# Optimization experiments

Measured on AMD Instinct MI355X. Metric: run time of the kernel, lower is better.

## Reference

```python
import jax, jax.numpy as jnp
import numpy as np

# quantization formats
E_Q, M_Q = 4, 3      # E4M3 fp8 for input/param quantizers
E_A, M_A = 5, 10     # fp16-like accumulate / output format


def quant(x, exp, man):
    """Round-to-nearest-even float quantization to (exp, man) bits,
    with subnormals and saturation (mptorch float_quantize semantics)."""
    ebias = 2 ** (exp - 1) - 1
    emin = 1 - ebias                      # min normal exponent
    maxv = (2.0 - 2.0 ** (-man)) * 2.0 ** ebias
    ax = jnp.abs(x)
    e = jnp.floor(jnp.log2(jnp.where(ax > 0, ax, 1.0)))
    e = jnp.maximum(e, emin)              # subnormal range shares emin scale
    scale = jnp.exp2(man - e)
    q = jnp.round(x * scale) / scale      # jnp.round is half-to-even
    return jnp.clip(q, -maxv, maxv)


def qgemm(x, wt, exp_add, man_add):
    """Custom-precision GEMM x[M,K] @ wt[K,N] with fma=True:
    the running accumulator is requantized to (exp_add, man_add)
    after every rank-1 (per-k) fused multiply-add."""
    M, K = x.shape
    N = wt.shape[1]

    def step(acc, xw):
        xk, wk = xw                       # [M], [N]
        acc = quant(acc + xk[:, None] * wk[None, :], exp_add, man_add)
        return acc, None

    acc0 = jnp.zeros((M, N), x.dtype)
    acc, _ = jax.lax.scan(step, acc0, (x.T, wt))
    return acc


def setup_inputs() -> dict:
    key = jax.random.key(0)
    k1, k2, k3 = jax.random.split(key, 3)
    in_f, out_f, m = 1024, 1024, 2048
    x = jax.random.normal(k1, (m, in_f), jnp.float32)
    weight = jax.random.normal(k2, (out_f, in_f), jnp.float32) / np.float32(np.sqrt(in_f))
    bound = 1.0 / np.float32(np.sqrt(in_f))
    bias = jax.random.uniform(k3, (out_f,), jnp.float32, -bound, bound)
    return {"x": x, "weight": weight, "bias": bias}


def reference(x, weight, bias):
    qx = quant(x, E_Q, M_Q)               # input_quant
    qw = quant(weight, E_Q, M_Q)          # param_quant
    qb = quant(bias, E_Q, M_Q)            # param_quant
    out = qgemm(qx, qw.T, E_A, M_A)       # float_gemm with fma accumulation
    out = out + qb[None, :]
    out = quant(out, E_A, M_A)            # output requantization
    return out
```

## Files before the change

kernel.cpp:

```cpp
#include <hip/hip_runtime.h>
#include <hip/hip_fp16.h>


#define M_DIM 2048
#define N_DIM 1024
#define K_DIM 1024

#define BM 64
#define BN 64
#define BK 64
#define NCHUNK (K_DIM / BK)

typedef unsigned u32;

__device__ __forceinline__ float quant_e4m3(float v) {
  unsigned au = __float_as_uint(v) & 0x7fffffffu;
  if (au == 0u) return v;
  int e = (int)(au >> 23) - 127;
  if (e < -6) e = -6;
  float s  = __uint_as_float((unsigned)(130 - e) << 23);
  float is = __uint_as_float((unsigned)(124 + e) << 23);
  float r = rintf(v * s) * is;
  return fminf(240.f, fmaxf(-240.f, r));
}

__global__ __launch_bounds__(256) void prep_kernel(const float* __restrict__ x,
                                                   const float* __restrict__ w,
                                                   u32* __restrict__ xP,
                                                   u32* __restrict__ wP) {
  __shared__ float tile[32][33];
  const int tx = threadIdx.x & 31;
  const int ty = threadIdx.x >> 5;
  if (blockIdx.x < 2048) {
    const int c0 = (blockIdx.x & 31) * 32;
    const int r0 = (blockIdx.x >> 5) * 32;
#pragma unroll
    for (int i = 0; i < 4; i++) {
      int r = r0 + ty + i * 8;
      tile[ty + i * 8][tx] = quant_e4m3(x[(size_t)r * K_DIM + c0 + tx]);
    }
    __syncthreads();
#pragma unroll
    for (int i = 0; i < 2; i++) {
      int tl = ty + i * 8;
      u32 lo = (u32)__half_as_ushort(__float2half(tile[tx][2 * tl]));
      u32 hi = (u32)__half_as_ushort(__float2half(tile[tx][2 * tl + 1]));
      xP[(size_t)(c0 / 2 + tl) * M_DIM + r0 + tx] = lo | (hi << 16);
    }
  } else {
    const int b = blockIdx.x - 2048;
    const int k0 = (b & 31) * 32;
    const int n0 = (b >> 5) * 32;
#pragma unroll
    for (int i = 0; i < 4; i++) {
      int n = n0 + ty + i * 8;
      tile[ty + i * 8][tx] = quant_e4m3(w[(size_t)n * K_DIM + k0 + tx]);
    }
    __syncthreads();
    const int tpl = threadIdx.x >> 4;
    const int npl = threadIdx.x & 15;
    u32 a0 = (u32)__half_as_ushort(__float2half(tile[2 * npl][2 * tpl])) |
             ((u32)__half_as_ushort(__float2half(tile[2 * npl + 1][2 * tpl])) << 16);
    u32 a1 = (u32)__half_as_ushort(__float2half(tile[2 * npl][2 * tpl + 1])) |
             ((u32)__half_as_ushort(__float2half(tile[2 * npl + 1][2 * tpl + 1])) << 16);
    uint2 o; o.x = a0; o.y = a1;
    *reinterpret_cast<uint2*>(wP + (size_t)(k0 / 2 + tpl) * N_DIM + n0 + 2 * npl) = o;
  }
}


__device__ __forceinline__ void gld16(const void* g, void* l) {
  __builtin_amdgcn_global_load_lds((const __attribute__((address_space(1))) u32*)g,
                                   (__attribute__((address_space(3))) u32*)l, 16, 0, 0);
}

__device__ __forceinline__ void pkfma_lo(u32& acc, u32 x, u32 w) {
  asm("v_pk_fma_f16 %0, %1, %2, %0 op_sel:[0,0,0] op_sel_hi:[0,1,1]"
      : "+v"(acc) : "v"(x), "v"(w));
}
__device__ __forceinline__ void pkfma_hi(u32& acc, u32 x, u32 w) {
  asm("v_pk_fma_f16 %0, %1, %2, %0 op_sel:[1,0,0] op_sel_hi:[1,1,1]"
      : "+v"(acc) : "v"(x), "v"(w));
}

__global__ __launch_bounds__(256, 2) void gemm_qfma(const u32* __restrict__ xP,
                                                    const u32* __restrict__ wP,
                                                    const float* __restrict__ b,
                                                    float* __restrict__ outp) {
  __shared__ __align__(16) u32 xs[2][BK / 2][BM];
  __shared__ __align__(16) u32 ws[2][BK / 2][BN];
  const int tid = threadIdx.x;
  const int lane = tid & 63;
  const int wv = tid >> 6;
  const int wr = wv >> 1;
  const int wc = wv & 1;
  const int tml = lane >> 3;
  const int tnl = lane & 7;
  const int bn0 = blockIdx.x * BN;
  const int bm0 = blockIdx.y * BM;
  const int xoff = wr * 32 + tml * 4;
  const int woff = wc * 32 + tnl * 4;

  u32 acc[4][2];
#pragma unroll
  for (int i = 0; i < 4; i++) { acc[i][0] = 0u; acc[i][1] = 0u; }

  const int srow = tid >> 4;
  const int scol = (tid & 15) << 2;
  const u32* xsrc = xP + (size_t)srow * M_DIM + bm0 + scol;
  const u32* wsrc = wP + (size_t)srow * N_DIM + bn0 + scol;

  auto stage = [&](int ch, int buf) {
    const u32* xp = xsrc + (size_t)ch * (BK / 2) * M_DIM;
    const u32* wp = wsrc + (size_t)ch * (BK / 2) * N_DIM;
    char* xl = (char*)&xs[buf][0][0] + tid * 16;
    char* wl = (char*)&ws[buf][0][0] + tid * 16;
    gld16(xp, xl);
    gld16(xp + (size_t)16 * M_DIM, xl + 4096);
    gld16(wp, wl);
    gld16(wp + (size_t)16 * N_DIM, wl + 4096);
  };

  auto compute = [&](int buf) {
#pragma unroll
    for (int tp = 0; tp < BK / 2; tp++) {
      const uint4 xv = *reinterpret_cast<const uint4*>(&xs[buf][tp][xoff]);
      const uint4 wv4 = *reinterpret_cast<const uint4*>(&ws[buf][tp][woff]);
      pkfma_lo(acc[0][0], xv.x, wv4.x); pkfma_lo(acc[0][1], xv.x, wv4.z);
      pkfma_lo(acc[1][0], xv.y, wv4.x); pkfma_lo(acc[1][1], xv.y, wv4.z);
      pkfma_lo(acc[2][0], xv.z, wv4.x); pkfma_lo(acc[2][1], xv.z, wv4.z);
      pkfma_lo(acc[3][0], xv.w, wv4.x); pkfma_lo(acc[3][1], xv.w, wv4.z);
      pkfma_hi(acc[0][0], xv.x, wv4.y); pkfma_hi(acc[0][1], xv.x, wv4.w);
      pkfma_hi(acc[1][0], xv.y, wv4.y); pkfma_hi(acc[1][1], xv.y, wv4.w);
      pkfma_hi(acc[2][0], xv.z, wv4.y); pkfma_hi(acc[2][1], xv.z, wv4.w);
      pkfma_hi(acc[3][0], xv.w, wv4.y); pkfma_hi(acc[3][1], xv.w, wv4.w);
    }
  };

  stage(0, 0);
  __syncthreads();
#pragma unroll 1
  for (int ch = 0; ch < NCHUNK; ch += 2) {
    stage(ch + 1, 1);
    compute(0);
    __syncthreads();
    if (ch + 2 < NCHUNK) stage(ch + 2, 0);
    compute(1);
    __syncthreads();
  }

  const int nc = bn0 + wc * 32 + tnl * 4;
  float4 bq;
  bq.x = quant_e4m3(b[nc + 0]);
  bq.y = quant_e4m3(b[nc + 1]);
  bq.z = quant_e4m3(b[nc + 2]);
  bq.w = quant_e4m3(b[nc + 3]);
#pragma unroll
  for (int i = 0; i < 4; i++) {
    __half2 a0 = *reinterpret_cast<__half2*>(&acc[i][0]);
    __half2 a1 = *reinterpret_cast<__half2*>(&acc[i][1]);
    float4 o;
    o.x = __half2float(__float2half(__low2float(a0)  + bq.x));
    o.y = __half2float(__float2half(__high2float(a0) + bq.y));
    o.z = __half2float(__float2half(__low2float(a1)  + bq.z));
    o.w = __half2float(__float2half(__high2float(a1) + bq.w));
    *reinterpret_cast<float4*>(
        outp + (size_t)(bm0 + wr * 32 + tml * 4 + i) * N_DIM + nc) = o;
  }
}

extern "C" void kernel_launch(void* const* d_in, const int* in_sizes, int n_in,
                              void* d_out, int out_size, void* d_ws, size_t ws_size,
                              hipStream_t stream) {
  const float* x = (const float*)d_in[0];
  const float* w = (const float*)d_in[1];
  const float* b = (const float*)d_in[2];
  float* outp = (float*)d_out;

  char* ws_ = (char*)d_ws;
  u32* xP = (u32*)ws_;
  u32* wP = (u32*)(ws_ + (size_t)(4 << 20));

  hipLaunchKernelGGL(prep_kernel, dim3(2048 + 1024), dim3(256), 0, stream,
                     x, w, xP, wP);
  hipLaunchKernelGGL(gemm_qfma, dim3(N_DIM / BN, M_DIM / BM), dim3(256), 0, stream,
                     xP, wP, b, outp);
}
```

Baseline: 110.3 us.

## Broadcast x operands through scalar registers and drop x from shared memory

Changes the packed layouts so each wave covers 16 rows of M and each lane one N column. x values become wave-uniform and are loaded with scalar loads straight from global into SGPRs, which are then used as the scalar operand of v_pk_fma_f16. Only the w tile is staged in LDS, as one dword per lane per k-pair. This removes the x LDS traffic and half the ds_read bandwidth. The risk is scalar-load latency sitting on the inner loop without prefetching, and column-strided scalar output stores in place of float4 stores.

```diff
diff --git a/kernel.cpp b/kernel.cpp
--- a/kernel.cpp
+++ b/kernel.cpp
@@ -12,6 +12,7 @@
 #define NCHUNK (K_DIM / BK)
 
 typedef unsigned u32;
+typedef u32 su16 __attribute__((ext_vector_type(16)));
 
 __device__ __forceinline__ float quant_e4m3(float v) {
   unsigned au = __float_as_uint(v) & 0x7fffffffu;
@@ -26,8 +27,8 @@
 
 __global__ __launch_bounds__(256) void prep_kernel(const float* __restrict__ x,
                                                    const float* __restrict__ w,
-                                                   u32* __restrict__ xP,
-                                                   u32* __restrict__ wP) {
+                                                   u32* __restrict__ xQ,
+                                                   u32* __restrict__ wK) {
   __shared__ float tile[32][33];
   const int tx = threadIdx.x & 31;
   const int ty = threadIdx.x >> 5;
@@ -43,9 +44,11 @@
 #pragma unroll
     for (int i = 0; i < 2; i++) {
       int tl = ty + i * 8;
-      u32 lo = (u32)__half_as_ushort(__float2half(tile[tx][2 * tl]));
-      u32 hi = (u32)__half_as_ushort(__float2half(tile[tx][2 * tl + 1]));
-      xP[(size_t)(c0 / 2 + tl) * M_DIM + r0 + tx] = lo | (hi << 16);
+      int mp = tx >> 1;
+      int j = tx & 1;
+      u32 lo = (u32)__half_as_ushort(__float2half(tile[2 * mp][2 * tl + j]));
+      u32 hi = (u32)__half_as_ushort(__float2half(tile[2 * mp + 1][2 * tl + j]));
+      xQ[(size_t)(c0 / 2 + tl) * M_DIM + r0 + tx] = lo | (hi << 16);
     }
   } else {
     const int b = blockIdx.x - 2048;
@@ -57,14 +60,13 @@
       tile[ty + i * 8][tx] = quant_e4m3(w[(size_t)n * K_DIM + k0 + tx]);
     }
     __syncthreads();
-    const int tpl = threadIdx.x >> 4;
-    const int npl = threadIdx.x & 15;
-    u32 a0 = (u32)__half_as_ushort(__float2half(tile[2 * npl][2 * tpl])) |
-             ((u32)__half_as_ushort(__float2half(tile[2 * npl + 1][2 * tpl])) << 16);
-    u32 a1 = (u32)__half_as_ushort(__float2half(tile[2 * npl][2 * tpl + 1])) |
-             ((u32)__half_as_ushort(__float2half(tile[2 * npl + 1][2 * tpl + 1])) << 16);
-    uint2 o; o.x = a0; o.y = a1;
-    *reinterpret_cast<uint2*>(wP + (size_t)(k0 / 2 + tpl) * N_DIM + n0 + 2 * npl) = o;
+#pragma unroll
+    for (int i = 0; i < 2; i++) {
+      int tl = ty + i * 8;
+      u32 lo = (u32)__half_as_ushort(__float2half(tile[tx][2 * tl]));
+      u32 hi = (u32)__half_as_ushort(__float2half(tile[tx][2 * tl + 1]));
+      wK[(size_t)(k0 / 2 + tl) * N_DIM + n0 + tx] = lo | (hi << 16);
+    }
   }
 }
 
@@ -74,66 +76,54 @@
                                    (__attribute__((address_space(3))) u32*)l, 16, 0, 0);
 }
 
-__device__ __forceinline__ void pkfma_lo(u32& acc, u32 x, u32 w) {
-  asm("v_pk_fma_f16 %0, %1, %2, %0 op_sel:[0,0,0] op_sel_hi:[0,1,1]"
-      : "+v"(acc) : "v"(x), "v"(w));
+__device__ __forceinline__ void pk_k0(u32& acc, u32 x, u32 w) {
+  asm("v_pk_fma_f16 %0, %1, %2, %0 op_sel:[0,0,0] op_sel_hi:[1,0,1]"
+      : "+v"(acc) : "s"(x), "v"(w));
 }
-__device__ __forceinline__ void pkfma_hi(u32& acc, u32 x, u32 w) {
-  asm("v_pk_fma_f16 %0, %1, %2, %0 op_sel:[1,0,0] op_sel_hi:[1,1,1]"
-      : "+v"(acc) : "v"(x), "v"(w));
+__device__ __forceinline__ void pk_k1(u32& acc, u32 x, u32 w) {
+  asm("v_pk_fma_f16 %0, %1, %2, %0 op_sel:[0,1,0] op_sel_hi:[1,1,1]"
+      : "+v"(acc) : "s"(x), "v"(w));
 }
 
-__global__ __launch_bounds__(256, 2) void gemm_qfma(const u32* __restrict__ xP,
-                                                    const u32* __restrict__ wP,
+__global__ __launch_bounds__(256, 2) void gemm_qfma(const u32* __restrict__ xQ,
+                                                    const u32* __restrict__ wK,
                                                     const float* __restrict__ b,
                                                     float* __restrict__ outp) {
-  __shared__ __align__(16) u32 xs[2][BK / 2][BM];
-  __shared__ __align__(16) u32 ws[2][BK / 2][BN];
+  __shared__ __align__(16) u32 wsh[2][BK / 2][BN];
   const int tid = threadIdx.x;
   const int lane = tid & 63;
-  const int wv = tid >> 6;
-  const int wr = wv >> 1;
-  const int wc = wv & 1;
-  const int tml = lane >> 3;
-  const int tnl = lane & 7;
+  const int uw = __builtin_amdgcn_readfirstlane(tid >> 6);
   const int bn0 = blockIdx.x * BN;
   const int bm0 = blockIdx.y * BM;
-  const int xoff = wr * 32 + tml * 4;
-  const int woff = wc * 32 + tnl * 4;
 
-  u32 acc[4][2];
+  u32 acc[8];
 #pragma unroll
-  for (int i = 0; i < 4; i++) { acc[i][0] = 0u; acc[i][1] = 0u; }
+  for (int i = 0; i < 8; i++) acc[i] = 0u;
 
-  const int srow = tid >> 4;
-  const int scol = (tid & 15) << 2;
-  const u32* xsrc = xP + (size_t)srow * M_DIM + bm0 + scol;
-  const u32* wsrc = wP + (size_t)srow * N_DIM + bn0 + scol;
-
+  const u32* wsrc = wK + (size_t)(tid >> 4) * N_DIM + bn0 + ((tid & 15) << 2);
   auto stage = [&](int ch, int buf) {
-    const u32* xp = xsrc + (size_t)ch * (BK / 2) * M_DIM;
     const u32* wp = wsrc + (size_t)ch * (BK / 2) * N_DIM;
-    char* xl = (char*)&xs[buf][0][0] + tid * 16;
-    char* wl = (char*)&ws[buf][0][0] + tid * 16;
-    gld16(xp, xl);
-    gld16(xp + (size_t)16 * M_DIM, xl + 4096);
+    char* wl = (char*)&wsh[buf][0][0] + tid * 16;
     gld16(wp, wl);
     gld16(wp + (size_t)16 * N_DIM, wl + 4096);
   };
 
-  auto compute = [&](int buf) {
+  const u32* const xw = xQ + bm0 + uw * 16;
+
+  auto compute = [&](int ch, int buf) {
 #pragma unroll
     for (int tp = 0; tp < BK / 2; tp++) {
-      const uint4 xv = *reinterpret_cast<const uint4*>(&xs[buf][tp][xoff]);
-      const uint4 wv4 = *reinterpret_cast<const uint4*>(&ws[buf][tp][woff]);
-      pkfma_lo(acc[0][0], xv.x, wv4.x); pkfma_lo(acc[0][1], xv.x, wv4.z);
-      pkfma_lo(acc[1][0], xv.y, wv4.x); pkfma_lo(acc[1][1], xv.y, wv4.z);
-      pkfma_lo(acc[2][0], xv.z, wv4.x); pkfma_lo(acc[2][1], xv.z, wv4.z);
-      pkfma_lo(acc[3][0], xv.w, wv4.x); pkfma_lo(acc[3][1], xv.w, wv4.z);
-      pkfma_hi(acc[0][0], xv.x, wv4.y); pkfma_hi(acc[0][1], xv.x, wv4.w);
-      pkfma_hi(acc[1][0], xv.y, wv4.y); pkfma_hi(acc[1][1], xv.y, wv4.w);
-      pkfma_hi(acc[2][0], xv.z, wv4.y); pkfma_hi(acc[2][1], xv.z, wv4.w);
-      pkfma_hi(acc[3][0], xv.w, wv4.y); pkfma_hi(acc[3][1], xv.w, wv4.w);
+      const su16 xv = *reinterpret_cast<const su16*>(
+          xw + (size_t)(ch * (BK / 2) + tp) * M_DIM);
+      const u32 wv = wsh[buf][tp][lane];
+      pk_k0(acc[0], xv[0],  wv); pk_k0(acc[1], xv[2],  wv);
+      pk_k0(acc[2], xv[4],  wv); pk_k0(acc[3], xv[6],  wv);
+      pk_k0(acc[4], xv[8],  wv); pk_k0(acc[5], xv[10], wv);
+      pk_k0(acc[6], xv[12], wv); pk_k0(acc[7], xv[14], wv);
+      pk_k1(acc[0], xv[1],  wv); pk_k1(acc[1], xv[3],  wv);
+      pk_k1(acc[2], xv[5],  wv); pk_k1(acc[3], xv[7],  wv);
+      pk_k1(acc[4], xv[9],  wv); pk_k1(acc[5], xv[11], wv);
+      pk_k1(acc[6], xv[13], wv); pk_k1(acc[7], xv[15], wv);
     }
   };
 
@@ -142,30 +132,21 @@
 #pragma unroll 1
   for (int ch = 0; ch < NCHUNK; ch += 2) {
     stage(ch + 1, 1);
-    compute(0);
+    compute(ch, 0);
     __syncthreads();
     if (ch + 2 < NCHUNK) stage(ch + 2, 0);
-    compute(1);
+    compute(ch + 1, 1);
     __syncthreads();
   }
 
-  const int nc = bn0 + wc * 32 + tnl * 4;
-  float4 bq;
-  bq.x = quant_e4m3(b[nc + 0]);
-  bq.y = quant_e4m3(b[nc + 1]);
-  bq.z = quant_e4m3(b[nc + 2]);
-  bq.w = quant_e4m3(b[nc + 3]);
+  const int nc = bn0 + lane;
+  const float bq = quant_e4m3(b[nc]);
+  float* orow = outp + (size_t)(bm0 + uw * 16) * N_DIM + nc;
 #pragma unroll
-  for (int i = 0; i < 4; i++) {
-    __half2 a0 = *reinterpret_cast<__half2*>(&acc[i][0]);
-    __half2 a1 = *reinterpret_cast<__half2*>(&acc[i][1]);
-    float4 o;
-    o.x = __half2float(__float2half(__low2float(a0)  + bq.x));
-    o.y = __half2float(__float2half(__high2float(a0) + bq.y));
-    o.z = __half2float(__float2half(__low2float(a1)  + bq.z));
-    o.w = __half2float(__float2half(__high2float(a1) + bq.w));
-    *reinterpret_cast<float4*>(
-        outp + (size_t)(bm0 + wr * 32 + tml * 4 + i) * N_DIM + nc) = o;
+  for (int mp = 0; mp < 8; mp++) {
+    __half2 a = *reinterpret_cast<__half2*>(&acc[mp]);
+    orow[(size_t)(2 * mp) * N_DIM]     = __half2float(__float2half(__low2float(a)  + bq));
+    orow[(size_t)(2 * mp + 1) * N_DIM] = __half2float(__float2half(__high2float(a) + bq));
   }
 }
 
@@ -178,11 +159,11 @@
   float* outp = (float*)d_out;
 
   char* ws_ = (char*)d_ws;
-  u32* xP = (u32*)ws_;
-  u32* wP = (u32*)(ws_ + (size_t)(4 << 20));
+  u32* xQ = (u32*)ws_;
+  u32* wK = (u32*)(ws_ + (size_t)(4 << 20));
 
   hipLaunchKernelGGL(prep_kernel, dim3(2048 + 1024), dim3(256), 0, stream,
-                     x, w, xP, wP);
+                     x, w, xQ, wK);
   hipLaunchKernelGGL(gemm_qfma, dim3(N_DIM / BN, M_DIM / BM), dim3(256), 0, stream,
-                     xP, wP, b, outp);
+                     xQ, wK, b, outp);
 }
```

New measurement: 207.8 us. +88.4%, slower.

## Retile GEMM to 32x128 blocks with 8x4 per-thread micro-tiles

Applied to the files above, without the earlier changes.

Changes the block tile from 64x64 with 256 threads to 32x128 with 128 threads, giving each thread an 8-row by 4-column accumulator tile. This raises packed-FMA work per shared-memory load and cuts LDS traffic per FMA. The staging loads are rearranged to match the new tile shapes. In exchange there are fewer waves per block and more registers per thread, which may reduce latency hiding.

```diff
diff --git a/kernel.cpp b/kernel.cpp
--- a/kernel.cpp
+++ b/kernel.cpp
@@ -6,8 +6,8 @@
 #define N_DIM 1024
 #define K_DIM 1024
 
-#define BM 64
-#define BN 64
+#define BM 32
+#define BN 128
 #define BK 64
 #define NCHUNK (K_DIM / BK)
 
@@ -83,57 +83,56 @@
       : "+v"(acc) : "v"(x), "v"(w));
 }
 
-__global__ __launch_bounds__(256, 2) void gemm_qfma(const u32* __restrict__ xP,
+__global__ __launch_bounds__(128, 2) void gemm_qfma(const u32* __restrict__ xP,
                                                     const u32* __restrict__ wP,
                                                     const float* __restrict__ b,
                                                     float* __restrict__ outp) {
   __shared__ __align__(16) u32 xs[2][BK / 2][BM];
-  __shared__ __align__(16) u32 ws[2][BK / 2][BN];
+  __shared__ __align__(16) u32 wsh[2][BK / 2][BN];
   const int tid = threadIdx.x;
-  const int lane = tid & 63;
-  const int wv = tid >> 6;
-  const int wr = wv >> 1;
-  const int wc = wv & 1;
-  const int tml = lane >> 3;
-  const int tnl = lane & 7;
+  const int tn = tid & 31;
+  const int tm = tid >> 5;
   const int bn0 = blockIdx.x * BN;
   const int bm0 = blockIdx.y * BM;
-  const int xoff = wr * 32 + tml * 4;
-  const int woff = wc * 32 + tnl * 4;
 
-  u32 acc[4][2];
+  u32 acc[8][2];
 #pragma unroll
-  for (int i = 0; i < 4; i++) { acc[i][0] = 0u; acc[i][1] = 0u; }
+  for (int i = 0; i < 8; i++) { acc[i][0] = 0u; acc[i][1] = 0u; }
 
-  const int srow = tid >> 4;
-  const int scol = (tid & 15) << 2;
-  const u32* xsrc = xP + (size_t)srow * M_DIM + bm0 + scol;
-  const u32* wsrc = wP + (size_t)srow * N_DIM + bn0 + scol;
+  const u32* xsrc = xP + (size_t)(tid >> 3) * M_DIM + bm0 + ((tid & 7) << 2);
+  const u32* wsrc = wP + (size_t)(tid >> 5) * N_DIM + bn0 + ((tid & 31) << 2);
 
   auto stage = [&](int ch, int buf) {
     const u32* xp = xsrc + (size_t)ch * (BK / 2) * M_DIM;
+    char* xl = (char*)&xs[buf][0][0] + tid * 16;
+    gld16(xp, xl);
+    gld16(xp + (size_t)16 * M_DIM, xl + 2048);
     const u32* wp = wsrc + (size_t)ch * (BK / 2) * N_DIM;
-    char* xl = (char*)&xs[buf][0][0] + tid * 16;
-    char* wl = (char*)&ws[buf][0][0] + tid * 16;
-    gld16(xp, xl);
-    gld16(xp + (size_t)16 * M_DIM, xl + 4096);
-    gld16(wp, wl);
-    gld16(wp + (size_t)16 * N_DIM, wl + 4096);
+    char* wl = (char*)&wsh[buf][0][0] + tid * 16;
+#pragma unroll
+    for (int p = 0; p < 8; p++)
+      gld16(wp + (size_t)(p * 4) * N_DIM, wl + p * 2048);
   };
 
   auto compute = [&](int buf) {
 #pragma unroll
     for (int tp = 0; tp < BK / 2; tp++) {
-      const uint4 xv = *reinterpret_cast<const uint4*>(&xs[buf][tp][xoff]);
-      const uint4 wv4 = *reinterpret_cast<const uint4*>(&ws[buf][tp][woff]);
-      pkfma_lo(acc[0][0], xv.x, wv4.x); pkfma_lo(acc[0][1], xv.x, wv4.z);
-      pkfma_lo(acc[1][0], xv.y, wv4.x); pkfma_lo(acc[1][1], xv.y, wv4.z);
-      pkfma_lo(acc[2][0], xv.z, wv4.x); pkfma_lo(acc[2][1], xv.z, wv4.z);
-      pkfma_lo(acc[3][0], xv.w, wv4.x); pkfma_lo(acc[3][1], xv.w, wv4.z);
-      pkfma_hi(acc[0][0], xv.x, wv4.y); pkfma_hi(acc[0][1], xv.x, wv4.w);
-      pkfma_hi(acc[1][0], xv.y, wv4.y); pkfma_hi(acc[1][1], xv.y, wv4.w);
-      pkfma_hi(acc[2][0], xv.z, wv4.y); pkfma_hi(acc[2][1], xv.z, wv4.w);
-      pkfma_hi(acc[3][0], xv.w, wv4.y); pkfma_hi(acc[3][1], xv.w, wv4.w);
+      u32 xm[8];
+      *reinterpret_cast<uint4*>(&xm[0]) =
+          *reinterpret_cast<const uint4*>(&xs[buf][tp][tm << 3]);
+      *reinterpret_cast<uint4*>(&xm[4]) =
+          *reinterpret_cast<const uint4*>(&xs[buf][tp][(tm << 3) + 4]);
+      const uint4 wv = *reinterpret_cast<const uint4*>(&wsh[buf][tp][tn << 2]);
+#pragma unroll
+      for (int i = 0; i < 8; i++) {
+        pkfma_lo(acc[i][0], xm[i], wv.x);
+        pkfma_lo(acc[i][1], xm[i], wv.z);
+      }
+#pragma unroll
+      for (int i = 0; i < 8; i++) {
+        pkfma_hi(acc[i][0], xm[i], wv.y);
+        pkfma_hi(acc[i][1], xm[i], wv.w);
+      }
     }
   };
 
@@ -149,14 +148,14 @@
     __syncthreads();
   }
 
-  const int nc = bn0 + wc * 32 + tnl * 4;
+  const int nc = bn0 + (tn << 2);
   float4 bq;
   bq.x = quant_e4m3(b[nc + 0]);
   bq.y = quant_e4m3(b[nc + 1]);
   bq.z = quant_e4m3(b[nc + 2]);
   bq.w = quant_e4m3(b[nc + 3]);
 #pragma unroll
-  for (int i = 0; i < 4; i++) {
+  for (int i = 0; i < 8; i++) {
     __half2 a0 = *reinterpret_cast<__half2*>(&acc[i][0]);
     __half2 a1 = *reinterpret_cast<__half2*>(&acc[i][1]);
     float4 o;
@@ -165,7 +164,7 @@
     o.z = __half2float(__float2half(__low2float(a1)  + bq.z));
     o.w = __half2float(__float2half(__high2float(a1) + bq.w));
     *reinterpret_cast<float4*>(
-        outp + (size_t)(bm0 + wr * 32 + tml * 4 + i) * N_DIM + nc) = o;
+        outp + (size_t)(bm0 + (tm << 3) + i) * N_DIM + nc) = o;
   }
 }
 
@@ -183,6 +182,6 @@
 
   hipLaunchKernelGGL(prep_kernel, dim3(2048 + 1024), dim3(256), 0, stream,
                      x, w, xP, wP);
-  hipLaunchKernelGGL(gemm_qfma, dim3(N_DIM / BN, M_DIM / BM), dim3(256), 0, stream,
+  hipLaunchKernelGGL(gemm_qfma, dim3(N_DIM / BN, M_DIM / BM), dim3(128), 0, stream,
                      xP, wP, b, outp);
 }
```

Result: slower. 145.8 us (+32.3%).
